# Optimization experiments

Measured on AMD Instinct MI355X. Metric: run time of the kernel, lower is better.

Reference implementation:

```python
import jax, jax.numpy as jnp
import numpy as np

B, L, W = 4096, 30, 5          # batch, MAX_TOKEN_LENGTH, WINDOW_SIZE
A, E = 30, 128                 # ALPHABET_SIZE, embedding dim
C = 40                         # OUT_CHANNELS
H, T = 128, 3                  # LSTM_UNITS, num CRF tags
LIN = W * C                    # 200
EPS = 1e-5


def setup_inputs():
    key = jax.random.key(0)
    ks = jax.random.split(key, 24)
    def rn(k, shape, s=0.1):
        return jax.random.normal(k, shape, jnp.float32) * s
    return {
        'x': jax.random.randint(ks[0], (B, L, W), 0, A, jnp.int32),
        'emb': rn(ks[1], (A, E), 1.0),
        'conv_w': rn(ks[2], (C, E, 3)),
        'conv_b': rn(ks[3], (C,)),
        'bn1_g': 1.0 + rn(ks[4], (C,)),
        'bn1_b': rn(ks[5], (C,)),
        'bn1_m': rn(ks[6], (C,)),
        'bn1_v': 0.5 + jax.random.uniform(ks[7], (C,), jnp.float32),
        'w_ih_f': rn(ks[8], (4 * H, LIN)),
        'w_hh_f': rn(ks[9], (4 * H, H)),
        'b_f': rn(ks[10], (4 * H,)),
        'w_ih_b': rn(ks[11], (4 * H, LIN)),
        'w_hh_b': rn(ks[12], (4 * H, H)),
        'b_b': rn(ks[13], (4 * H,)),
        'bn2_g': 1.0 + rn(ks[14], (2 * H,)),
        'bn2_b': rn(ks[15], (2 * H,)),
        'bn2_m': rn(ks[16], (2 * H,)),
        'bn2_v': 0.5 + jax.random.uniform(ks[17], (2 * H,), jnp.float32),
        'fc_w': rn(ks[18], (T, 2 * H)),
        'fc_b': rn(ks[19], (T,)),
        'trans': rn(ks[20], (T, T)),
        'start_t': rn(ks[21], (T,)),
        'end_t': rn(ks[22], (T,)),
    }


def _lstm_dir(seq, w_ih, w_hh, b, reverse):
    # seq: [B, L, F]; torch gate order i, f, g, o
    xs = jnp.einsum('blf,gf->lbg', seq, w_ih) + b  # [L, B, 4H]
    h0 = jnp.zeros((seq.shape[0], H), seq.dtype)
    def step(carry, xt):
        h, c = carry
        z = xt + h @ w_hh.T
        i, f, g, o = jnp.split(z, 4, axis=-1)
        c = jax.nn.sigmoid(f) * c + jax.nn.sigmoid(i) * jnp.tanh(g)
        h = jax.nn.sigmoid(o) * jnp.tanh(c)
        return (h, c), h
    _, hs = jax.lax.scan(step, (h0, h0), xs, reverse=reverse)
    return hs.transpose(1, 0, 2)  # [B, L, H]


def _viterbi(emis, mask, trans, start_t, end_t):
    # emis: [B, L, T], mask: [B, L] bool
    score = start_t + emis[:, 0]                      # [B, T]
    def step(score, inp):
        e_t, m_t = inp                                # [B, T], [B]
        cand = score[:, :, None] + trans              # [B, Tprev, Tnext]
        ptr = jnp.argmax(cand, axis=1)                # [B, T]
        new = jnp.max(cand, axis=1) + e_t
        return jnp.where(m_t[:, None], new, score), ptr
    score, hist = jax.lax.scan(
        step, score, (emis[:, 1:].transpose(1, 0, 2), mask[:, 1:].T))
    score = score + end_t
    best = jnp.max(score, axis=1)                     # [B] path scores
    last = jnp.argmax(score, axis=1)                  # [B]
    def back(tag, inp):
        h_t, m_t = inp
        prev = jnp.take_along_axis(h_t, tag[:, None], axis=1)[:, 0]
        tag = jnp.where(m_t, prev, tag)
        return tag, tag
    _, ys = jax.lax.scan(back, last, (hist, mask[:, 1:].T), reverse=True)
    tags = jnp.concatenate([ys, last[None]], axis=0).T  # [B, L]
    return best, tags


def reference(x, emb, conv_w, conv_b, bn1_g, bn1_b, bn1_m, bn1_v,
              w_ih_f, w_hh_f, b_f, w_ih_b, w_hh_b, b_b,
              bn2_g, bn2_b, bn2_m, bn2_v, fc_w, fc_b, trans, start_t, end_t):
    mask = x[:, :, 2] > 0                             # [B, L]
    e = emb[x.reshape(B * L, W)]                      # [N, W, E]  (dropout=eval noop)
    e = e.transpose(0, 2, 1)                          # [N, E, W]
    y = jax.lax.conv_general_dilated(
        e, conv_w, (1,), [(1, 1)],
        dimension_numbers=('NCH', 'OIH', 'NCH')) + conv_b[:, None]
    # BatchNorm1d (inference, running stats)
    y = (y - bn1_m[:, None]) * (bn1_g / jnp.sqrt(bn1_v + EPS))[:, None] + bn1_b[:, None]
    y = jax.nn.relu(y)
    # MaxPool1d(k=3, stride=1, pad=1): length preserved
    y = jax.lax.reduce_window(y, -jnp.inf, jax.lax.max,
                              (1, 1, 3), (1, 1, 1),
                              [(0, 0), (0, 0), (1, 1)])
    y = y.reshape(B, L, LIN)                          # torch.flatten is channel-major = row-major reshape
    hf = _lstm_dir(y, w_ih_f, w_hh_f, b_f, False)
    hb = _lstm_dir(y, w_ih_b, w_hh_b, b_b, True)
    h = jnp.concatenate([hf, hb], axis=-1)            # [B, L, 2H]
    h = (h - bn2_m) * (bn2_g / jnp.sqrt(bn2_v + EPS)) + bn2_b
    emis = h @ fc_w.T + fc_b                          # [B, L, T]
    return _viterbi(emis, mask, trans, start_t, end_t)
```

## Files before the change

kernel.cpp:

```cpp
#include <hip/hip_runtime.h>
#include <math.h>

#define BB    4096
#define LL    30
#define WW    5
#define CC    40
#define HH    128
#define TT    3
#define KA    328
#define NB    32
#define NT_   1024
#define FSTR  232
#define HSTR  136
#define CW    1056

#define WS_P    0
#define WS_BC   3600
#define WS_BG   3648
#define WS_WFC  4672
#define WS_EB   5440
#define WS_WBF  5504
#define WS_EMIS (5504 + 540672)

typedef __bf16 bf16x8 __attribute__((ext_vector_type(8)));
typedef float  f32x4  __attribute__((ext_vector_type(4)));
typedef unsigned short u16x8 __attribute__((ext_vector_type(8)));

__device__ __forceinline__ float sigm(float x) {
    return __builtin_amdgcn_rcpf(1.0f + __expf(-x));
}
__device__ __forceinline__ float tanh_fast(float x) {
    return 2.0f * __builtin_amdgcn_rcpf(1.0f + __expf(-2.0f * x)) - 1.0f;
}
__device__ __forceinline__ unsigned short f2bf(float f) {
    unsigned u = __builtin_bit_cast(unsigned, f);
    return (unsigned short)((u + 0x7FFFu + ((u >> 16) & 1u)) >> 16);
}
__device__ __forceinline__ float bf2f(unsigned short h) {
    unsigned u = ((unsigned)h) << 16;
    return __builtin_bit_cast(float, u);
}

__global__ void prep_kernel(const float* __restrict__ emb, const float* __restrict__ conv_w,
                            const float* __restrict__ conv_b,
                            const float* __restrict__ bn1_g, const float* __restrict__ bn1_b,
                            const float* __restrict__ bn1_m, const float* __restrict__ bn1_v,
                            const float* __restrict__ w_ih_f, const float* __restrict__ w_hh_f,
                            const float* __restrict__ b_f,
                            const float* __restrict__ w_ih_b, const float* __restrict__ w_hh_b,
                            const float* __restrict__ b_b,
                            const float* __restrict__ bn2_g, const float* __restrict__ bn2_b,
                            const float* __restrict__ bn2_m, const float* __restrict__ bn2_v,
                            const float* __restrict__ fc_w, const float* __restrict__ fc_b,
                            float* __restrict__ ws)
{
    const int gid = blockIdx.x * blockDim.x + threadIdx.x;
    const int gsz = gridDim.x * blockDim.x;

    for (int idx = gid; idx < 3600; idx += gsz) {
        int k = idx / 1200, rem = idx % 1200, a = rem / 40, c = rem % 40;
        float s1 = bn1_g[c] / sqrtf(bn1_v[c] + 1e-5f);
        float acc = 0.f;
        for (int e = 0; e < 128; ++e)
            acc += emb[a * 128 + e] * conv_w[(c * 128 + e) * 3 + k];
        ws[WS_P + idx] = acc * s1;
    }
    for (int c = gid; c < CC; c += gsz) {
        float s1 = bn1_g[c] / sqrtf(bn1_v[c] + 1e-5f);
        ws[WS_BC + c] = (conv_b[c] - bn1_m[c]) * s1 + bn1_b[c];
    }
    for (int i = gid; i < 1024; i += gsz) {
        int d = i >> 9, g = i & 511;
        ws[WS_BG + i] = d ? b_b[g] : b_f[g];
    }
    for (int i = gid; i < 768; i += gsz) {
        int d = i / 384, r = i % 384, t = r / 128, u = r % 128;
        int j = d * 128 + u;
        float s2 = bn2_g[j] / sqrtf(bn2_v[j] + 1e-5f);
        ws[WS_WFC + i] = fc_w[t * 256 + j] * s2;
    }
    for (int t = gid; t < TT; t += gsz) {
        float acc = fc_b[t];
        for (int j = 0; j < 256; ++j) {
            float s2 = bn2_g[j] / sqrtf(bn2_v[j] + 1e-5f);
            acc += fc_w[t * 256 + j] * (bn2_b[j] - bn2_m[j] * s2);
        }
        ws[WS_EB + t] = acc;
    }
    unsigned short* wsu = (unsigned short*)ws;
    for (int i = gid; i < 2 * 512 * CW; i += gsz) {
        int d = i / (512 * CW), r = i % (512 * CW);
        int n = r / CW, q = r % CW;
        int Ks = q / 96, t = q % 96, s = t / 32, k32 = t % 32;
        int k = Ks * 32 + k32;
        int u = n >> 2, g = n & 3, row = g * 128 + u;
        const float* wih = d ? w_ih_b : w_ih_f;
        const float* whh = d ? w_hh_b : w_hh_f;
        float w = (k < 200) ? wih[row * 200 + k]
                            : ((k >= 224) ? whh[row * 128 + (k - 224)] : 0.f);
        unsigned short t0 = f2bf(w);
        float r1 = w - bf2f(t0);
        unsigned short t1 = f2bf(r1);
        unsigned short t2 = f2bf(r1 - bf2f(t1));
        wsu[2 * WS_WBF + i] = (s == 0) ? t0 : ((s == 1) ? t1 : t2);
    }
}

__global__ __launch_bounds__(1024, 1)
void lstm_kernel(const int* __restrict__ x, float* __restrict__ ws)
{
    __shared__ unsigned short Fh[2][NB * FSTR], Fl[2][NB * FSTR], Fm[2][NB * FSTR];
    __shared__ unsigned short Hh[NB * HSTR], Hl[NB * HSTR], Hm[NB * HSTR];
    __shared__ float Pp_s[3600];
    __shared__ float Wfc_s[384];
    __shared__ float biasC_s[40];

    const int tid = threadIdx.x;
    const int d   = blockIdx.x & 1;
    const int b0  = (blockIdx.x >> 1) * NB;

    const unsigned short* __restrict__ Wb =
        (const unsigned short*)ws + 2 * WS_WBF + d * (512 * CW);
    float* emis = ws + WS_EMIS + d * (BB * LL * TT);

    for (int i = tid; i < 3600; i += NT_) Pp_s[i] = ws[WS_P + i];
    for (int i = tid; i < 384;  i += NT_) Wfc_s[i] = ws[WS_WFC + d * 384 + i];
    for (int i = tid; i < 40;   i += NT_) biasC_s[i] = ws[WS_BC + i];
    for (int i = tid; i < NB * FSTR; i += NT_) {
        ((unsigned*)Fh)[i] = 0u; ((unsigned*)Fl)[i] = 0u; ((unsigned*)Fm)[i] = 0u;
    }
    for (int i = tid; i < NB * HSTR / 2; i += NT_) {
        ((unsigned*)Hh)[i] = 0u; ((unsigned*)Hl)[i] = 0u; ((unsigned*)Hm)[i] = 0u;
    }

    const int lane = tid & 63;
    const int wv   = tid >> 6;
    const bool is_gemm = (wv < 8);
    const int quad = lane >> 4;
    const int ml   = lane & 15;

    const int gw = wv & 7;
    const unsigned short* __restrict__ Wn0 = Wb + (gw * 64 +  0 + ml) * CW + quad * 8;
    const unsigned short* __restrict__ Wn1 = Wb + (gw * 64 + 16 + ml) * CW + quad * 8;
    const unsigned short* __restrict__ Wn2 = Wb + (gw * 64 + 32 + ml) * CW + quad * 8;
    const unsigned short* __restrict__ Wn3 = Wb + (gw * 64 + 48 + ml) * CW + quad * 8;

    const float* bgp = ws + WS_BG + d * 512;
    int   un[4];
    float bIv[4], bFv[4], bGv[4], bOv[4];
    #pragma unroll
    for (int nt = 0; nt < 4; ++nt) {
        int u = gw * 16 + nt * 4 + quad;
        un[nt]  = u;
        bIv[nt] = bgp[u];
        bFv[nt] = bgp[128 + u];
        bGv[nt] = bgp[256 + u];
        bOv[nt] = bgp[384 + u];
    }
    float cst[2][4];
    #pragma unroll
    for (int mt = 0; mt < 2; ++mt)
        #pragma unroll
        for (int nt = 0; nt < 4; ++nt) cst[mt][nt] = 0.f;

    const int atid = tid - 512;

    __syncthreads();

#define DO_FEATURES(LPOS, BUF)                                                 \
    for (int p = atid; p < NB * CC; p += 512) {                                \
        int bb = p / CC, c = p % CC;                                           \
        const int* tok = x + (((b0 + bb) * LL) + (LPOS)) * WW;                 \
        int t0 = tok[0], t1 = tok[1], t2 = tok[2], t3 = tok[3], t4 = tok[4];   \
        float bc = biasC_s[c];                                                 \
        float a0 = bc + Pp_s[(30 + t0) * 40 + c] + Pp_s[(60 + t1) * 40 + c];   \
        float a1 = bc + Pp_s[t0 * 40 + c] + Pp_s[(30 + t1) * 40 + c] + Pp_s[(60 + t2) * 40 + c]; \
        float a2 = bc + Pp_s[t1 * 40 + c] + Pp_s[(30 + t2) * 40 + c] + Pp_s[(60 + t3) * 40 + c]; \
        float a3 = bc + Pp_s[t2 * 40 + c] + Pp_s[(30 + t3) * 40 + c] + Pp_s[(60 + t4) * 40 + c]; \
        float a4 = bc + Pp_s[t3 * 40 + c] + Pp_s[(30 + t4) * 40 + c];          \
        a0 = fmaxf(a0, 0.f); a1 = fmaxf(a1, 0.f); a2 = fmaxf(a2, 0.f);         \
        a3 = fmaxf(a3, 0.f); a4 = fmaxf(a4, 0.f);                              \
        float f[5];                                                            \
        f[0] = fmaxf(a0, a1);                                                  \
        f[1] = fmaxf(fmaxf(a0, a1), a2);                                       \
        f[2] = fmaxf(fmaxf(a1, a2), a3);                                       \
        f[3] = fmaxf(fmaxf(a2, a3), a4);                                       \
        f[4] = fmaxf(a3, a4);                                                  \
        int base = bb * FSTR + c * 5;                                          \
        _Pragma("unroll")                                                      \
        for (int j = 0; j < 5; ++j) {                                          \
            unsigned short h0 = f2bf(f[j]);                                    \
            float r1 = f[j] - bf2f(h0);                                        \
            unsigned short h1 = f2bf(r1);                                      \
            unsigned short h2 = f2bf(r1 - bf2f(h1));                           \
            Fh[BUF][base + j] = h0;                                            \
            Fl[BUF][base + j] = h1;                                            \
            Fm[BUF][base + j] = h2;                                            \
        }                                                                      \
    }

    if (!is_gemm) {
        const int l0 = d ? (LL - 1) : 0;
        DO_FEATURES(l0, 0)
    }
    __syncthreads();

    f32x4 acc[2][4];

    for (int step = 0; step < LL; ++step) {
        const int fb = step & 1;

        if (is_gemm) {
            #pragma unroll
            for (int mt = 0; mt < 2; ++mt)
                #pragma unroll
                for (int nt = 0; nt < 4; ++nt)
                    acc[mt][nt] = (f32x4){0.f, 0.f, 0.f, 0.f};

#define WLOAD(B, P, KS)                                                        \
            {                                                                  \
                B[0] = *(const bf16x8*)((P) + (KS) * 96);                      \
                B[1] = *(const bf16x8*)((P) + (KS) * 96 + 32);                 \
                B[2] = *(const bf16x8*)((P) + (KS) * 96 + 64);                 \
            }
#define GEMM6(B, NT)                                                           \
            {                                                                  \
                acc[0][NT] = __builtin_amdgcn_mfma_f32_16x16x32_bf16(B[0], a0[0], acc[0][NT], 0, 0, 0); \
                acc[0][NT] = __builtin_amdgcn_mfma_f32_16x16x32_bf16(B[0], a0[1], acc[0][NT], 0, 0, 0); \
                acc[0][NT] = __builtin_amdgcn_mfma_f32_16x16x32_bf16(B[1], a0[0], acc[0][NT], 0, 0, 0); \
                acc[0][NT] = __builtin_amdgcn_mfma_f32_16x16x32_bf16(B[1], a0[1], acc[0][NT], 0, 0, 0); \
                acc[0][NT] = __builtin_amdgcn_mfma_f32_16x16x32_bf16(B[2], a0[0], acc[0][NT], 0, 0, 0); \
                acc[0][NT] = __builtin_amdgcn_mfma_f32_16x16x32_bf16(B[0], a0[2], acc[0][NT], 0, 0, 0); \
                acc[1][NT] = __builtin_amdgcn_mfma_f32_16x16x32_bf16(B[0], a1[0], acc[1][NT], 0, 0, 0); \
                acc[1][NT] = __builtin_amdgcn_mfma_f32_16x16x32_bf16(B[0], a1[1], acc[1][NT], 0, 0, 0); \
                acc[1][NT] = __builtin_amdgcn_mfma_f32_16x16x32_bf16(B[1], a1[0], acc[1][NT], 0, 0, 0); \
                acc[1][NT] = __builtin_amdgcn_mfma_f32_16x16x32_bf16(B[1], a1[1], acc[1][NT], 0, 0, 0); \
                acc[1][NT] = __builtin_amdgcn_mfma_f32_16x16x32_bf16(B[2], a1[0], acc[1][NT], 0, 0, 0); \
                acc[1][NT] = __builtin_amdgcn_mfma_f32_16x16x32_bf16(B[0], a1[2], acc[1][NT], 0, 0, 0); \
            }
            {
                bf16x8 bufA[3], bufB[3];
                WLOAD(bufA, Wn0, 0)

                #pragma unroll
                for (int Ks = 0; Ks < 11; ++Ks) {
                    bf16x8 a0[3], a1[3];
                    if (Ks < 7) {
                        const int ko = Ks * 32 + quad * 8;
                        a0[0] = *(const bf16x8*)&Fh[fb][ml * FSTR + ko];
                        a0[1] = *(const bf16x8*)&Fl[fb][ml * FSTR + ko];
                        a0[2] = *(const bf16x8*)&Fm[fb][ml * FSTR + ko];
                        a1[0] = *(const bf16x8*)&Fh[fb][(16 + ml) * FSTR + ko];
                        a1[1] = *(const bf16x8*)&Fl[fb][(16 + ml) * FSTR + ko];
                        a1[2] = *(const bf16x8*)&Fm[fb][(16 + ml) * FSTR + ko];
                    } else {
                        const int ko = (Ks - 7) * 32 + quad * 8;
                        a0[0] = *(const bf16x8*)&Hh[ml * HSTR + ko];
                        a0[1] = *(const bf16x8*)&Hl[ml * HSTR + ko];
                        a0[2] = *(const bf16x8*)&Hm[ml * HSTR + ko];
                        a1[0] = *(const bf16x8*)&Hh[(16 + ml) * HSTR + ko];
                        a1[1] = *(const bf16x8*)&Hl[(16 + ml) * HSTR + ko];
                        a1[2] = *(const bf16x8*)&Hm[(16 + ml) * HSTR + ko];
                    }
                    WLOAD(bufB, Wn1, Ks)
                    GEMM6(bufA, 0)
                    WLOAD(bufA, Wn2, Ks)
                    GEMM6(bufB, 1)
                    WLOAD(bufB, Wn3, Ks)
                    GEMM6(bufA, 2)
                    if (Ks < 10) WLOAD(bufA, Wn0, Ks + 1)
                    GEMM6(bufB, 3)
                }
            }
#undef WLOAD
#undef GEMM6
        } else {
            if (step + 1 < LL) {
                const int lnext = d ? (LL - 2 - step) : (step + 1);
                DO_FEATURES(lnext, (step + 1) & 1)
            }
            if (step > 0 && atid < 192) {
                const int lprev = d ? (LL - step) : (step - 1);
                int bb = atid / 6, r6 = atid % 6, t = r6 >> 1, seg = r6 & 1;
                int hb = bb * HSTR + seg * 64;
                const float* wfc = &Wfc_s[t * 128 + seg * 64];
                float s = 0.f;
                #pragma unroll
                for (int i = 0; i < 8; ++i) {
                    u16x8 v0 = *(const u16x8*)&Hh[hb + i * 8];
                    u16x8 v1 = *(const u16x8*)&Hl[hb + i * 8];
                    u16x8 v2 = *(const u16x8*)&Hm[hb + i * 8];
                    #pragma unroll
                    for (int j = 0; j < 8; ++j) {
                        float h = bf2f(v0[j]) + bf2f(v1[j]) + bf2f(v2[j]);
                        s += h * wfc[i * 8 + j];
                    }
                }
                s += __shfl_xor(s, 1);
                if (seg == 0)
                    emis[(((b0 + bb) * LL) + lprev) * TT + t] = s;
            }
        }

        __syncthreads();

        if (is_gemm) {
            #pragma unroll
            for (int mt = 0; mt < 2; ++mt) {
                #pragma unroll
                for (int nt = 0; nt < 4; ++nt) {
                    float zi = acc[mt][nt][0] + bIv[nt];
                    float zf = acc[mt][nt][1] + bFv[nt];
                    float zg = acc[mt][nt][2] + bGv[nt];
                    float zo = acc[mt][nt][3] + bOv[nt];
                    float cn = sigm(zf) * cst[mt][nt] + sigm(zi) * tanh_fast(zg);
                    cst[mt][nt] = cn;
                    float h = sigm(zo) * tanh_fast(cn);
                    unsigned short h0 = f2bf(h);
                    float r1 = h - bf2f(h0);
                    unsigned short h1 = f2bf(r1);
                    unsigned short h2 = f2bf(r1 - bf2f(h1));
                    int idx = (mt * 16 + ml) * HSTR + un[nt];
                    Hh[idx] = h0;
                    Hl[idx] = h1;
                    Hm[idx] = h2;
                }
            }
        }
        __syncthreads();
    }

    if (!is_gemm && atid < 192) {
        const int llast = d ? 0 : (LL - 1);
        int bb = atid / 6, r6 = atid % 6, t = r6 >> 1, seg = r6 & 1;
        int hb = bb * HSTR + seg * 64;
        const float* wfc = &Wfc_s[t * 128 + seg * 64];
        float s = 0.f;
        #pragma unroll
        for (int i = 0; i < 8; ++i) {
            u16x8 v0 = *(const u16x8*)&Hh[hb + i * 8];
            u16x8 v1 = *(const u16x8*)&Hl[hb + i * 8];
            u16x8 v2 = *(const u16x8*)&Hm[hb + i * 8];
            #pragma unroll
            for (int j = 0; j < 8; ++j) {
                float h = bf2f(v0[j]) + bf2f(v1[j]) + bf2f(v2[j]);
                s += h * wfc[i * 8 + j];
            }
        }
        s += __shfl_xor(s, 1);
        if (seg == 0)
            emis[(((b0 + bb) * LL) + llast) * TT + t] = s;
    }
#undef DO_FEATURES
}

__global__ void viterbi_kernel(const int* __restrict__ x, const float* __restrict__ ws,
                               const float* __restrict__ trans,
                               const float* __restrict__ start_t,
                               const float* __restrict__ end_t,
                               float* __restrict__ out)
{
    int b = blockIdx.x * blockDim.x + threadIdx.x;
    if (b >= BB) return;
    const float* eF = ws + WS_EMIS;
    const float* eB = ws + WS_EMIS + BB * LL * TT;
    const float eb0 = ws[WS_EB + 0], eb1 = ws[WS_EB + 1], eb2 = ws[WS_EB + 2];
    float tr[9];
    #pragma unroll
    for (int i = 0; i < 9; ++i) tr[i] = trans[i];

    int base = b * LL * TT;
    float s0 = start_t[0] + eF[base + 0] + eB[base + 0] + eb0;
    float s1 = start_t[1] + eF[base + 1] + eB[base + 1] + eb1;
    float s2 = start_t[2] + eF[base + 2] + eB[base + 2] + eb2;

    unsigned hist[LL - 1];
    unsigned maskbits = 0;

    #pragma unroll
    for (int l = 1; l < LL; ++l) {
        bool m = x[(b * LL + l) * WW + 2] > 0;
        if (m) maskbits |= (1u << l);
        int idx = base + l * TT;
        float e0 = eF[idx + 0] + eB[idx + 0] + eb0;
        float e1 = eF[idx + 1] + eB[idx + 1] + eb1;
        float e2 = eF[idx + 2] + eB[idx + 2] + eb2;

        float ns[3]; int pt[3];
        #pragma unroll
        for (int nt = 0; nt < 3; ++nt) {
            float c0 = s0 + tr[0 * 3 + nt];
            float c1 = s1 + tr[1 * 3 + nt];
            float c2 = s2 + tr[2 * 3 + nt];
            int p = 0; float bc = c0;
            if (c1 > bc) { bc = c1; p = 1; }
            if (c2 > bc) { bc = c2; p = 2; }
            ns[nt] = bc; pt[nt] = p;
        }
        ns[0] += e0; ns[1] += e1; ns[2] += e2;
        hist[l - 1] = (unsigned)pt[0] | ((unsigned)pt[1] << 2) | ((unsigned)pt[2] << 4);
        if (m) { s0 = ns[0]; s1 = ns[1]; s2 = ns[2]; }
    }
    s0 += end_t[0]; s1 += end_t[1]; s2 += end_t[2];
    float best = s0; int last = 0;
    if (s1 > best) { best = s1; last = 1; }
    if (s2 > best) { best = s2; last = 2; }

    out[b] = best;
    float* tags = out + BB + b * LL;
    int tag = last;
    tags[LL - 1] = (float)last;
    #pragma unroll
    for (int l = LL - 1; l >= 1; --l) {
        int prev = (int)((hist[l - 1] >> (2 * tag)) & 3u);
        if (maskbits & (1u << l)) tag = prev;
        tags[l - 1] = (float)tag;
    }
}

extern "C" void kernel_launch(void* const* d_in, const int* in_sizes, int n_in,
                              void* d_out, int out_size, void* d_ws, size_t ws_size,
                              hipStream_t stream)
{
    const int*   x      = (const int*)  d_in[0];
    const float* emb    = (const float*)d_in[1];
    const float* conv_w = (const float*)d_in[2];
    const float* conv_b = (const float*)d_in[3];
    const float* bn1_g  = (const float*)d_in[4];
    const float* bn1_b  = (const float*)d_in[5];
    const float* bn1_m  = (const float*)d_in[6];
    const float* bn1_v  = (const float*)d_in[7];
    const float* w_ih_f = (const float*)d_in[8];
    const float* w_hh_f = (const float*)d_in[9];
    const float* b_f    = (const float*)d_in[10];
    const float* w_ih_b = (const float*)d_in[11];
    const float* w_hh_b = (const float*)d_in[12];
    const float* b_b    = (const float*)d_in[13];
    const float* bn2_g  = (const float*)d_in[14];
    const float* bn2_b  = (const float*)d_in[15];
    const float* bn2_m  = (const float*)d_in[16];
    const float* bn2_v  = (const float*)d_in[17];
    const float* fc_w   = (const float*)d_in[18];
    const float* fc_b   = (const float*)d_in[19];
    const float* trans  = (const float*)d_in[20];
    const float* start_t= (const float*)d_in[21];
    const float* end_t  = (const float*)d_in[22];

    float* ws  = (float*)d_ws;
    float* out = (float*)d_out;

    prep_kernel<<<256, 256, 0, stream>>>(emb, conv_w, conv_b,
                                         bn1_g, bn1_b, bn1_m, bn1_v,
                                         w_ih_f, w_hh_f, b_f,
                                         w_ih_b, w_hh_b, b_b,
                                         bn2_g, bn2_b, bn2_m, bn2_v,
                                         fc_w, fc_b, ws);
    lstm_kernel<<<256, 1024, 0, stream>>>(x, ws);
    viterbi_kernel<<<16, 256, 0, stream>>>(x, ws, trans, start_t, end_t, out);
}
```

Measured before the change: 798.6 us.

## Halve LSTM block to 512 threads with 4 GEMM waves each covering 128 gate columns

The LSTM block shrinks from 1024 to 512 threads. Four MFMA waves now each compute 8 N-tiles of 16 gate columns instead of eight waves computing 4, and four auxiliary waves take over feature building and emission work. The MFMA sequence is also interleaved between the two M-tiles, and gate biases are reloaded inside the epilogue rather than held in registers. The aim is to cut per-step barrier cost and let each wave reuse its A fragments across more tiles, at the cost of more accumulator registers and less latency hiding per step.

```diff
diff --git a/kernel.cpp b/kernel.cpp
--- a/kernel.cpp
+++ b/kernel.cpp
@@ -9,7 +9,7 @@
 #define TT    3
 #define KA    328
 #define NB    32
-#define NT_   1024
+#define NT_   512
 #define FSTR  232
 #define HSTR  136
 #define CW    1056
@@ -106,7 +106,7 @@
     }
 }
 
-__global__ __launch_bounds__(1024, 1)
+__global__ __launch_bounds__(512, 1)
 void lstm_kernel(const int* __restrict__ x, float* __restrict__ ws)
 {
     __shared__ unsigned short Fh[2][NB * FSTR], Fl[2][NB * FSTR], Fm[2][NB * FSTR];
@@ -135,40 +135,30 @@
 
     const int lane = tid & 63;
     const int wv   = tid >> 6;
-    const bool is_gemm = (wv < 8);
+    const bool is_gemm = (wv < 4);
     const int quad = lane >> 4;
     const int ml   = lane & 15;
 
-    const int gw = wv & 7;
-    const unsigned short* __restrict__ Wn0 = Wb + (gw * 64 +  0 + ml) * CW + quad * 8;
-    const unsigned short* __restrict__ Wn1 = Wb + (gw * 64 + 16 + ml) * CW + quad * 8;
-    const unsigned short* __restrict__ Wn2 = Wb + (gw * 64 + 32 + ml) * CW + quad * 8;
-    const unsigned short* __restrict__ Wn3 = Wb + (gw * 64 + 48 + ml) * CW + quad * 8;
+    const int gw = wv & 3;
+    const unsigned short* __restrict__ Wn[8];
+    #pragma unroll
+    for (int nt = 0; nt < 8; ++nt)
+        Wn[nt] = Wb + (gw * 128 + nt * 16 + ml) * CW + quad * 8;
 
     const float* bgp = ws + WS_BG + d * 512;
-    int   un[4];
-    float bIv[4], bFv[4], bGv[4], bOv[4];
-    #pragma unroll
-    for (int nt = 0; nt < 4; ++nt) {
-        int u = gw * 16 + nt * 4 + quad;
-        un[nt]  = u;
-        bIv[nt] = bgp[u];
-        bFv[nt] = bgp[128 + u];
-        bGv[nt] = bgp[256 + u];
-        bOv[nt] = bgp[384 + u];
-    }
-    float cst[2][4];
+
+    float cst[2][8];
     #pragma unroll
     for (int mt = 0; mt < 2; ++mt)
         #pragma unroll
-        for (int nt = 0; nt < 4; ++nt) cst[mt][nt] = 0.f;
-
-    const int atid = tid - 512;
+        for (int nt = 0; nt < 8; ++nt) cst[mt][nt] = 0.f;
+
+    const int atid = tid - 256;
 
     __syncthreads();
 
 #define DO_FEATURES(LPOS, BUF)                                                 \
-    for (int p = atid; p < NB * CC; p += 512) {                                \
+    for (int p = atid; p < NB * CC; p += 256) {                                \
         int bb = p / CC, c = p % CC;                                           \
         const int* tok = x + (((b0 + bb) * LL) + (LPOS)) * WW;                 \
         int t0 = tok[0], t1 = tok[1], t2 = tok[2], t3 = tok[3], t4 = tok[4];   \
@@ -205,7 +195,7 @@
     }
     __syncthreads();
 
-    f32x4 acc[2][4];
+    f32x4 acc[2][8];
 
     for (int step = 0; step < LL; ++step) {
         const int fb = step & 1;
@@ -214,7 +204,7 @@
             #pragma unroll
             for (int mt = 0; mt < 2; ++mt)
                 #pragma unroll
-                for (int nt = 0; nt < 4; ++nt)
+                for (int nt = 0; nt < 8; ++nt)
                     acc[mt][nt] = (f32x4){0.f, 0.f, 0.f, 0.f};
 
 #define WLOAD(B, P, KS)                                                        \
@@ -226,21 +216,21 @@
 #define GEMM6(B, NT)                                                           \
             {                                                                  \
                 acc[0][NT] = __builtin_amdgcn_mfma_f32_16x16x32_bf16(B[0], a0[0], acc[0][NT], 0, 0, 0); \
+                acc[1][NT] = __builtin_amdgcn_mfma_f32_16x16x32_bf16(B[0], a1[0], acc[1][NT], 0, 0, 0); \
                 acc[0][NT] = __builtin_amdgcn_mfma_f32_16x16x32_bf16(B[0], a0[1], acc[0][NT], 0, 0, 0); \
+                acc[1][NT] = __builtin_amdgcn_mfma_f32_16x16x32_bf16(B[0], a1[1], acc[1][NT], 0, 0, 0); \
                 acc[0][NT] = __builtin_amdgcn_mfma_f32_16x16x32_bf16(B[1], a0[0], acc[0][NT], 0, 0, 0); \
+                acc[1][NT] = __builtin_amdgcn_mfma_f32_16x16x32_bf16(B[1], a1[0], acc[1][NT], 0, 0, 0); \
                 acc[0][NT] = __builtin_amdgcn_mfma_f32_16x16x32_bf16(B[1], a0[1], acc[0][NT], 0, 0, 0); \
+                acc[1][NT] = __builtin_amdgcn_mfma_f32_16x16x32_bf16(B[1], a1[1], acc[1][NT], 0, 0, 0); \
                 acc[0][NT] = __builtin_amdgcn_mfma_f32_16x16x32_bf16(B[2], a0[0], acc[0][NT], 0, 0, 0); \
+                acc[1][NT] = __builtin_amdgcn_mfma_f32_16x16x32_bf16(B[2], a1[0], acc[1][NT], 0, 0, 0); \
                 acc[0][NT] = __builtin_amdgcn_mfma_f32_16x16x32_bf16(B[0], a0[2], acc[0][NT], 0, 0, 0); \
-                acc[1][NT] = __builtin_amdgcn_mfma_f32_16x16x32_bf16(B[0], a1[0], acc[1][NT], 0, 0, 0); \
-                acc[1][NT] = __builtin_amdgcn_mfma_f32_16x16x32_bf16(B[0], a1[1], acc[1][NT], 0, 0, 0); \
-                acc[1][NT] = __builtin_amdgcn_mfma_f32_16x16x32_bf16(B[1], a1[0], acc[1][NT], 0, 0, 0); \
-                acc[1][NT] = __builtin_amdgcn_mfma_f32_16x16x32_bf16(B[1], a1[1], acc[1][NT], 0, 0, 0); \
-                acc[1][NT] = __builtin_amdgcn_mfma_f32_16x16x32_bf16(B[2], a1[0], acc[1][NT], 0, 0, 0); \
                 acc[1][NT] = __builtin_amdgcn_mfma_f32_16x16x32_bf16(B[0], a1[2], acc[1][NT], 0, 0, 0); \
             }
             {
                 bf16x8 bufA[3], bufB[3];
-                WLOAD(bufA, Wn0, 0)
+                WLOAD(bufA, Wn[0], 0)
 
                 #pragma unroll
                 for (int Ks = 0; Ks < 11; ++Ks) {
@@ -262,14 +252,22 @@
                         a1[1] = *(const bf16x8*)&Hl[(16 + ml) * HSTR + ko];
                         a1[2] = *(const bf16x8*)&Hm[(16 + ml) * HSTR + ko];
                     }
-                    WLOAD(bufB, Wn1, Ks)
+                    WLOAD(bufB, Wn[1], Ks)
                     GEMM6(bufA, 0)
-                    WLOAD(bufA, Wn2, Ks)
+                    WLOAD(bufA, Wn[2], Ks)
                     GEMM6(bufB, 1)
-                    WLOAD(bufB, Wn3, Ks)
+                    WLOAD(bufB, Wn[3], Ks)
                     GEMM6(bufA, 2)
-                    if (Ks < 10) WLOAD(bufA, Wn0, Ks + 1)
+                    WLOAD(bufA, Wn[4], Ks)
                     GEMM6(bufB, 3)
+                    WLOAD(bufB, Wn[5], Ks)
+                    GEMM6(bufA, 4)
+                    WLOAD(bufA, Wn[6], Ks)
+                    GEMM6(bufB, 5)
+                    WLOAD(bufB, Wn[7], Ks)
+                    GEMM6(bufA, 6)
+                    if (Ks < 10) WLOAD(bufA, Wn[0], Ks + 1)
+                    GEMM6(bufB, 7)
                 }
             }
 #undef WLOAD
@@ -306,13 +304,16 @@
 
         if (is_gemm) {
             #pragma unroll
-            for (int mt = 0; mt < 2; ++mt) {
+            for (int nt = 0; nt < 8; ++nt) {
+                const int u = gw * 32 + nt * 4 + quad;
+                const float bI = bgp[u], bF = bgp[128 + u];
+                const float bG = bgp[256 + u], bO = bgp[384 + u];
                 #pragma unroll
-                for (int nt = 0; nt < 4; ++nt) {
-                    float zi = acc[mt][nt][0] + bIv[nt];
-                    float zf = acc[mt][nt][1] + bFv[nt];
-                    float zg = acc[mt][nt][2] + bGv[nt];
-                    float zo = acc[mt][nt][3] + bOv[nt];
+                for (int mt = 0; mt < 2; ++mt) {
+                    float zi = acc[mt][nt][0] + bI;
+                    float zf = acc[mt][nt][1] + bF;
+                    float zg = acc[mt][nt][2] + bG;
+                    float zo = acc[mt][nt][3] + bO;
                     float cn = sigm(zf) * cst[mt][nt] + sigm(zi) * tanh_fast(zg);
                     cst[mt][nt] = cn;
                     float h = sigm(zo) * tanh_fast(cn);
@@ -320,7 +321,7 @@
                     float r1 = h - bf2f(h0);
                     unsigned short h1 = f2bf(r1);
                     unsigned short h2 = f2bf(r1 - bf2f(h1));
-                    int idx = (mt * 16 + ml) * HSTR + un[nt];
+                    int idx = (mt * 16 + ml) * HSTR + u;
                     Hh[idx] = h0;
                     Hl[idx] = h1;
                     Hm[idx] = h2;
@@ -455,6 +456,6 @@
                                          w_ih_b, w_hh_b, b_b,
                                          bn2_g, bn2_b, bn2_m, bn2_v,
                                          fc_w, fc_b, ws);
-    lstm_kernel<<<256, 1024, 0, stream>>>(x, ws);
+    lstm_kernel<<<256, 512, 0, stream>>>(x, ws);
     viterbi_kernel<<<16, 256, 0, stream>>>(x, ws, trans, start_t, end_t, out);
 }
```

After: 872.9 us. +9.3%, slower.
